# Kernel optimization log

Hardware: AMD Instinct MI355X
Metric: run time of the kernel (lower is better)

The kernel has to match this reference:

```python
import jax, jax.numpy as jnp
import numpy as np

HIDDEN = 512
B, H, W = 8, 48, 48
SCALE = 1.0 / np.sqrt(HIDDEN).astype(np.float32)


def conv1x1(x, w, b):
    # x: [B, C, H, W], w: [O, C], b: [O]  (1x1 Conv2d == channel matmul)
    return jnp.einsum('bchw,oc->bohw', x, w) + b[None, :, None, None]


def setup_inputs() -> dict:
    key = jax.random.key(0)
    ks = jax.random.split(key, 10)
    s = 1.0 / np.sqrt(HIDDEN)
    return {
        'locx': jax.random.normal(ks[0], (B, HIDDEN, H, W), dtype=jnp.float32),
        'glox': jax.random.normal(ks[1], (B, HIDDEN, H, W), dtype=jnp.float32),
        'Wq': jax.random.normal(ks[2], (HIDDEN, HIDDEN), dtype=jnp.float32) * s,
        'bq': jax.random.normal(ks[3], (HIDDEN,), dtype=jnp.float32) * 0.01,
        'Wk': jax.random.normal(ks[4], (HIDDEN, HIDDEN), dtype=jnp.float32) * s,
        'bk': jax.random.normal(ks[5], (HIDDEN,), dtype=jnp.float32) * 0.01,
        'Wv': jax.random.normal(ks[6], (HIDDEN, HIDDEN), dtype=jnp.float32) * s,
        'bv': jax.random.normal(ks[7], (HIDDEN,), dtype=jnp.float32) * 0.01,
        'Wo': jax.random.normal(ks[8], (HIDDEN, HIDDEN), dtype=jnp.float32) * s,
        'bo': jax.random.normal(ks[9], (HIDDEN,), dtype=jnp.float32) * 0.01,
    }


def reference(locx, glox, Wq, bq, Wk, bk, Wv, bv, Wo, bo):
    b, c, h, w = locx.shape
    # 1x1 conv projections
    q = conv1x1(locx, Wq, bq).reshape(b, c, h * w)   # [B, C, N]
    k = conv1x1(glox, Wk, bk).reshape(b, c, -1)      # [B, C, M]
    v = conv1x1(glox, Wv, bv).reshape(b, c, -1)      # [B, C, M]
    # scores = Q^T K / sqrt(hidden)  -> [B, N, M]
    scores = jnp.einsum('bcn,bcm->bnm', q, k) * SCALE
    probs = jax.nn.softmax(scores, axis=-1)           # dropout rate 0.0 -> identity
    # context = probs @ V^T -> [B, N, C] -> [B, C, H, H]
    ctx = jnp.einsum('bnm,bcm->bcn', probs, v).reshape(b, c, h, h)
    out = conv1x1(ctx, Wo, bo)                        # proj dropout 0.0 -> identity
    return out
```

## Files before the change

kernel.cpp:

```cpp
#include <hip/hip_runtime.h>
#include <hip/hip_bf16.h>

typedef __attribute__((ext_vector_type(4))) float f32x4;
typedef __attribute__((ext_vector_type(8))) short bf16x8;
typedef __attribute__((ext_vector_type(4))) short s16x4;

#define C_DIM 512
#define N_PIX 2304
#define N_BATCH 8
#define ATT_SCALE 0.04419417382415922f
#define NJB 9

typedef __attribute__((address_space(3))) unsigned int lds_u32;
typedef const __attribute__((address_space(1))) unsigned int glob_u32;

__device__ __forceinline__ void gl2lds16(const __hip_bfloat16* g, __hip_bfloat16* l)
{
    __builtin_amdgcn_global_load_lds((glob_u32*)g, (lds_u32*)l, 16, 0, 0);
}


#define BAR()  __builtin_amdgcn_s_barrier()
#define LGK0() asm volatile("s_waitcnt lgkmcnt(0)" ::: "memory")
#define VM4()  asm volatile("s_waitcnt vmcnt(4)" ::: "memory")
#define VM0()  asm volatile("s_waitcnt vmcnt(0)" ::: "memory")
#define PRIO(p) __builtin_amdgcn_s_setprio(p)

#define STAGE_A(dd, hh, tk) do { \
    _Pragma("unroll") \
    for (int ss = 0; ss < 2; ++ss) { \
        const int ur0 = wave * 16 + ss * 8; \
        const int row0 = ((ur0 >> 6) << 7) + (hh) * 64 + (ur0 & 63); \
        gl2lds16(gA + (size_t)row0 * C_DIM + (tk) * 64, \
                 (__hip_bfloat16*)&LA[dd][row0 * 64]); \
    } } while (0)

#define STAGE_B(dd, bb, tk) do { \
    _Pragma("unroll") \
    for (int ss = 0; ss < 2; ++ss) { \
        const int ur0 = wave * 16 + ss * 8; \
        const int row0 = ((ur0 >> 5) << 6) + (bb) * 32 + (ur0 & 31); \
        gl2lds16(gB + (size_t)row0 * C_DIM + (tk) * 64, \
                 (__hip_bfloat16*)&LB[dd][row0 * 64]); \
    } } while (0)

#define LOAD_A(dd, hh) do { \
    _Pragma("unroll") \
    for (int tt = 0; tt < 4; ++tt) { \
        const int rb = (wr * 128 + (hh) * 64 + tt * 16 + fr) * 64; \
        _Pragma("unroll") \
        for (int kk = 0; kk < 2; ++kk) \
            aF[tt][kk] = *(const bf16x8*)(&LA[dd][rb + (((kk * 4 + fq) ^ sw) << 3)]); \
    } } while (0)

#define LOAD_B(dd, bb, dst) do { \
    _Pragma("unroll") \
    for (int s2 = 0; s2 < 2; ++s2) { \
        const int rb = (wc * 64 + (bb) * 32 + s2 * 16 + fr) * 64; \
        _Pragma("unroll") \
        for (int kk = 0; kk < 2; ++kk) \
            dst[s2][kk] = *(const bf16x8*)(&LB[dd][rb + (((kk * 4 + fq) ^ sw) << 3)]); \
    } } while (0)

#define MFMA_Q(HH, BB, bsrc) do { \
    _Pragma("unroll") \
    for (int tt = 0; tt < 4; ++tt) \
    _Pragma("unroll") \
    for (int s2 = 0; s2 < 2; ++s2) \
    _Pragma("unroll") \
    for (int kk = 0; kk < 2; ++kk) \
        acc[(HH) * 4 + tt][(BB) * 2 + s2] = __builtin_amdgcn_mfma_f32_16x16x32_bf16( \
            aF[tt][kk], bsrc[s2][kk], acc[(HH) * 4 + tt][(BB) * 2 + s2], 0, 0, 0); \
    } while (0)

template<int NS>
__global__ __launch_bounds__(512, 2)
void s_vp(const __hip_bfloat16* __restrict__ Qt, const __hip_bfloat16* __restrict__ Kt,
          __hip_bfloat16* __restrict__ Pu, float* __restrict__ rp,
          const __hip_bfloat16* __restrict__ wo, const __hip_bfloat16* __restrict__ Vt,
          __hip_bfloat16* __restrict__ Vp, int bz_off, long sPu)
{
    __shared__ __hip_bfloat16 LA[2][256 * 64];
    __shared__ __hip_bfloat16 LB[2][256 * 64];

    const int lin = blockIdx.x;
    const int bz  = lin % NS + bz_off;
    const int t   = lin / NS;
    const bool is_s = (t < 81);

    int ib, jb;
    const __hip_bfloat16 *A, *B;
    __hip_bfloat16* D;
    const long sQ = (long)N_PIX * C_DIM;
    if (is_s) {
        ib = t / 9; jb = t % 9;
        A = Qt + (size_t)bz * sQ;
        B = Kt + (size_t)bz * sQ;
        D = Pu + (size_t)bz * (size_t)sPu;
    } else {
        int u = t - 81;
        ib = u / 9; jb = u % 9;
        A = wo;
        B = Vt + (size_t)bz * sQ;
        D = Vp + (size_t)bz * sQ;
    }
    const int i0 = ib * 256;
    const int j0 = jb * 256;

    const int tid  = threadIdx.x;
    const int lane = tid & 63;
    const int wave = tid >> 6;

    const int lrow = lane >> 3;
    const int lcs  = (lane & 7) ^ lrow;
    const __hip_bfloat16* gA = A + (size_t)(i0 + lrow) * C_DIM + lcs * 8;
    const __hip_bfloat16* gB = B + (size_t)(j0 + lrow) * C_DIM + lcs * 8;

    const int fr = lane & 15;
    const int fq = lane >> 4;
    const int sw = fr & 7;
    const int wr = wave >> 2;
    const int wc = wave & 3;

    f32x4 acc[8][4];
#pragma unroll
    for (int a = 0; a < 8; ++a)
#pragma unroll
        for (int b = 0; b < 4; ++b)
            acc[a][b] = (f32x4){0.f, 0.f, 0.f, 0.f};

    bf16x8 aF[4][2], bF0[2][2], bF1[2][2];

    STAGE_A(0, 0, 0); STAGE_B(0, 0, 0); STAGE_B(0, 1, 0); STAGE_A(0, 1, 0);
    STAGE_A(1, 0, 1); STAGE_B(1, 1, 1);
    VM4();
    BAR();

    for (int kt = 0; kt < 6; ++kt) {
        const int d = kt & 1, e = d ^ 1;
        LOAD_A(d, 0); LOAD_B(d, 0, bF0);
        STAGE_A(e, 1, kt + 1);
        BAR(); LGK0();
        PRIO(1); MFMA_Q(0, 0, bF0); PRIO(0);
        BAR();
        LOAD_B(d, 1, bF1);
        STAGE_B(e, 0, kt + 1);
        BAR(); LGK0();
        PRIO(1); MFMA_Q(0, 1, bF1); PRIO(0);
        BAR();
        LOAD_A(d, 1);
        STAGE_A(d, 0, kt + 2);
        BAR(); LGK0();
        PRIO(1); MFMA_Q(1, 1, bF1); PRIO(0);
        BAR();
        STAGE_B(d, 1, kt + 2);
        VM4();
        BAR();
        PRIO(1); MFMA_Q(1, 0, bF0); PRIO(0);
        BAR();
    }
    {
        LOAD_A(0, 0); LOAD_B(0, 0, bF0);
        STAGE_A(1, 1, 7);
        BAR(); LGK0();
        PRIO(1); MFMA_Q(0, 0, bF0); PRIO(0);
        BAR();
        LOAD_B(0, 1, bF1);
        STAGE_B(1, 0, 7);
        BAR(); LGK0();
        PRIO(1); MFMA_Q(0, 1, bF1); PRIO(0);
        BAR();
        LOAD_A(0, 1);
        BAR(); LGK0();
        PRIO(1); MFMA_Q(1, 1, bF1); PRIO(0);
        BAR();
        VM0();
        BAR();
        PRIO(1); MFMA_Q(1, 0, bF0); PRIO(0);
        BAR();
    }
    {
        LOAD_A(1, 0); LOAD_B(1, 0, bF0);
        BAR(); LGK0();
        PRIO(1); MFMA_Q(0, 0, bF0); PRIO(0);
        BAR();
        LOAD_B(1, 1, bF1);
        BAR(); LGK0();
        PRIO(1); MFMA_Q(0, 1, bF1); PRIO(0);
        BAR();
        LOAD_A(1, 1);
        BAR(); LGK0();
        PRIO(1); MFMA_Q(1, 1, bF1); PRIO(0);
        BAR();
        PRIO(1); MFMA_Q(1, 0, bF0); PRIO(0);
    }

    if (is_s) {
        float rpart[8][4];
#pragma unroll
        for (int a = 0; a < 8; ++a)
#pragma unroll
            for (int r = 0; r < 4; ++r)
                rpart[a][r] = 0.f;
#pragma unroll
        for (int a = 0; a < 8; ++a) {
            const int grow = i0 + wr * 128 + a * 16 + fq * 4;
#pragma unroll
            for (int b = 0; b < 4; ++b) {
                const int col = j0 + wc * 64 + b * 16 + fr;
#pragma unroll
                for (int r = 0; r < 4; ++r) {
                    float v = __expf(acc[a][b][r] * ATT_SCALE);
                    rpart[a][r] += v;
                    D[(size_t)(grow + r) * N_PIX + col] = __float2bfloat16(v);
                }
            }
        }
#pragma unroll
        for (int m = 1; m < 16; m <<= 1)
#pragma unroll
            for (int a = 0; a < 8; ++a)
#pragma unroll
                for (int r = 0; r < 4; ++r)
                    rpart[a][r] += __shfl_xor(rpart[a][r], m);
        float* rsl = (float*)&LA[0][0];
        __syncthreads();
        if (fr == 0) {
#pragma unroll
            for (int a = 0; a < 8; ++a)
#pragma unroll
                for (int r = 0; r < 4; ++r)
                    rsl[wave * 128 + a * 16 + fq * 4 + r] = rpart[a][r];
        }
        __syncthreads();
        if (tid < 256) {
            const int wr2 = tid >> 7, rl = tid & 127;
            float s = rsl[(wr2 * 4 + 0) * 128 + rl] + rsl[(wr2 * 4 + 1) * 128 + rl]
                    + rsl[(wr2 * 4 + 2) * 128 + rl] + rsl[(wr2 * 4 + 3) * 128 + rl];
            rp[((size_t)jb * N_BATCH + bz) * N_PIX + i0 + tid] = s;
        }
    } else {
#pragma unroll
        for (int a = 0; a < 8; ++a) {
            const int grow = i0 + wr * 128 + a * 16 + fq * 4;
#pragma unroll
            for (int b = 0; b < 4; ++b) {
                const int col = j0 + wc * 64 + b * 16 + fr;
#pragma unroll
                for (int r = 0; r < 4; ++r)
                    D[(size_t)(grow + r) * N_PIX + col] = __float2bfloat16(acc[a][b][r]);
            }
        }
    }
}

#undef STAGE_A
#undef STAGE_B
#undef LOAD_A
#undef LOAD_B
#undef MFMA_Q
#undef BAR
#undef LGK0
#undef VM4
#undef VM0
#undef PRIO

template<int NS>
__global__ __launch_bounds__(256)
void pv_out(const __hip_bfloat16* __restrict__ Vp, const __hip_bfloat16* __restrict__ Pu,
            float* __restrict__ out, const float* __restrict__ bo,
            const float* __restrict__ rp, int bz_off, long sPu)
{
    __shared__ __hip_bfloat16 As[64 * 64];
    __shared__ __hip_bfloat16 Bs[128 * 64];

    const int lin = blockIdx.x;
    const int bz  = lin % NS + bz_off;
    const int t   = lin / NS;
    const int ib  = t % 8;
    const int jb  = t / 8;
    const int i0  = ib * 64;
    const int j0  = jb * 128;

    const long sCN = (long)C_DIM * N_PIX;
    const __hip_bfloat16* A = Vp + (size_t)bz * sCN;
    const __hip_bfloat16* B = Pu + (size_t)bz * (size_t)sPu;
    float* D = out + (size_t)bz * sCN;

    const int tid  = threadIdx.x;
    const int lane = tid & 63;
    const int wave = tid >> 6;

    const int lrow = lane >> 3;
    const int lcs  = (lane & 7) ^ lrow;
    const __hip_bfloat16* ga = A + (size_t)(i0 + wave * 16 + lrow) * N_PIX + lcs * 8;
    const __hip_bfloat16* gb = B + (size_t)(j0 + wave * 32 + lrow) * N_PIX + lcs * 8;
    __hip_bfloat16* la = As + wave * 16 * 64;
    __hip_bfloat16* lb = Bs + wave * 32 * 64;

    const int fr = lane & 15;
    const int fq = lane >> 4;
    const int sw = fr & 7;
    const int wi = (wave >> 1) * 32;
    const int wj = (wave & 1) * 64;

    f32x4 acc[2][4];
#pragma unroll
    for (int a = 0; a < 2; ++a)
#pragma unroll
        for (int b = 0; b < 4; ++b)
            acc[a][b] = (f32x4){0.f, 0.f, 0.f, 0.f};

    for (int k0 = 0; k0 < N_PIX; k0 += 64) {
#pragma unroll
        for (int ss = 0; ss < 2; ++ss)
            gl2lds16(ga + (size_t)ss * 8 * N_PIX + k0, la + ss * 8 * 64);
#pragma unroll
        for (int ss = 0; ss < 4; ++ss)
            gl2lds16(gb + (size_t)ss * 8 * N_PIX + k0, lb + ss * 8 * 64);
        __syncthreads();

#pragma unroll
        for (int kk = 0; kk < 2; ++kk) {
            bf16x8 af[2], bfr[4];
            const int ca = ((kk * 4 + fq) ^ sw) << 3;
#pragma unroll
            for (int tt = 0; tt < 2; ++tt)
                af[tt]  = *(const bf16x8*)(&As[(wi + tt * 16 + fr) * 64 + ca]);
#pragma unroll
            for (int tt = 0; tt < 4; ++tt)
                bfr[tt] = *(const bf16x8*)(&Bs[(wj + tt * 16 + fr) * 64 + ca]);
#pragma unroll
            for (int a = 0; a < 2; ++a)
#pragma unroll
                for (int b = 0; b < 4; ++b)
                    acc[a][b] = __builtin_amdgcn_mfma_f32_16x16x32_bf16(
                        af[a], bfr[b], acc[a][b], 0, 0, 0);
        }
        __syncthreads();
    }

    const int orow = fq * 4;
    float rjv[4];
#pragma unroll
    for (int b = 0; b < 4; ++b) {
        int j = j0 + wj + b * 16 + fr;
        float s = 0.f;
#pragma unroll
        for (int jj = 0; jj < NJB; ++jj)
            s += rp[((size_t)jj * N_BATCH + bz) * N_PIX + j];
        rjv[b] = 1.f / s;
    }

#pragma unroll
    for (int a = 0; a < 2; ++a) {
        int ibx = i0 + wi + a * 16 + orow;
#pragma unroll
        for (int r = 0; r < 4; ++r) {
            float bi = bo[ibx + r];
#pragma unroll
            for (int b = 0; b < 4; ++b) {
                int j = j0 + wj + b * 16 + fr;
                D[(size_t)(ibx + r) * N_PIX + j] = acc[a][b][r] * rjv[b] + bi;
            }
        }
    }
}

__global__ __launch_bounds__(256)
void proj_qkv(const __hip_bfloat16* __restrict__ Xl,
              const __hip_bfloat16* __restrict__ Xg,
              const __hip_bfloat16* __restrict__ wgt,
              const float* __restrict__ bq, const float* __restrict__ bk,
              const float* __restrict__ bv,
              __hip_bfloat16* __restrict__ QKV)
{
    __shared__ __hip_bfloat16 As[128 * 64];
    __shared__ __hip_bfloat16 Bs[128 * 64];

    const int lin = blockIdx.x;
    const int s   = lin % 24;
    const int bz  = s & 7;
    const int mat = s >> 3;
    const int t   = lin / 24;
    const int j0  = (t & 3) * 128;
    const int i0  = (t >> 2) * 128;

    const __hip_bfloat16* Ab = ((mat == 0) ? Xl : Xg) + (size_t)bz * N_PIX * C_DIM;
    const __hip_bfloat16* Bb = wgt + (size_t)mat * C_DIM * C_DIM;
    const float* bias = (mat == 0) ? bq : (mat == 1) ? bk : bv;
    __hip_bfloat16* D = QKV + ((size_t)mat * N_BATCH + bz) * N_PIX * C_DIM;

    const int tid  = threadIdx.x;
    const int lane = tid & 63;
    const int wave = tid >> 6;

    const int lrow = lane >> 3;
    const int lcs  = (lane & 7) ^ lrow;
    const __hip_bfloat16* ga = Ab + (size_t)(i0 + wave * 32 + lrow) * C_DIM + lcs * 8;
    const __hip_bfloat16* gb = Bb + (size_t)(j0 + wave * 32 + lrow) * C_DIM + lcs * 8;
    __hip_bfloat16* la = As + wave * 32 * 64;
    __hip_bfloat16* lb = Bs + wave * 32 * 64;

    const int fr = lane & 15;
    const int fq = lane >> 4;
    const int sw = fr & 7;
    const int wi = (wave >> 1) * 64;
    const int wj = (wave & 1) * 64;

    f32x4 acc[4][4];
#pragma unroll
    for (int a = 0; a < 4; ++a)
#pragma unroll
        for (int b = 0; b < 4; ++b)
            acc[a][b] = (f32x4){0.f, 0.f, 0.f, 0.f};

    for (int k0 = 0; k0 < C_DIM; k0 += 64) {
#pragma unroll
        for (int ss = 0; ss < 4; ++ss) {
            gl2lds16(ga + (size_t)ss * 8 * C_DIM + k0, la + ss * 8 * 64);
            gl2lds16(gb + (size_t)ss * 8 * C_DIM + k0, lb + ss * 8 * 64);
        }
        __syncthreads();

#pragma unroll
        for (int kk = 0; kk < 2; ++kk) {
            bf16x8 af[4], bfr[4];
            const int ca = ((kk * 4 + fq) ^ sw) << 3;
#pragma unroll
            for (int tt = 0; tt < 4; ++tt) {
                af[tt]  = *(const bf16x8*)(&As[(wi + tt * 16 + fr) * 64 + ca]);
                bfr[tt] = *(const bf16x8*)(&Bs[(wj + tt * 16 + fr) * 64 + ca]);
            }
#pragma unroll
            for (int a = 0; a < 4; ++a)
#pragma unroll
                for (int b = 0; b < 4; ++b)
                    acc[a][b] = __builtin_amdgcn_mfma_f32_16x16x32_bf16(
                        af[a], bfr[b], acc[a][b], 0, 0, 0);
        }
        __syncthreads();
    }

    const int orow = fq * 4;
#pragma unroll
    for (int a = 0; a < 4; ++a) {
        int ibx = i0 + wi + a * 16 + orow;
#pragma unroll
        for (int b = 0; b < 4; ++b) {
            int j = j0 + wj + b * 16 + fr;
            float bj = bias[j];
#pragma unroll
            for (int r = 0; r < 4; ++r)
                D[(size_t)(ibx + r) * C_DIM + j] = __float2bfloat16(acc[a][b][r] + bj);
        }
    }
}

__global__ __launch_bounds__(256)
void prep(const float* __restrict__ locx, const float* __restrict__ glox,
          __hip_bfloat16* __restrict__ Xl, __hip_bfloat16* __restrict__ Xg,
          const float* __restrict__ w0, const float* __restrict__ w1,
          const float* __restrict__ w2, const float* __restrict__ w3,
          __hip_bfloat16* __restrict__ wgt)
{
    const int lin = blockIdx.x;
    const int tid = threadIdx.x;

    if (lin < 4608) {
        __shared__ float t[64 * 65];
        const int z  = lin & 15;
        const int t2 = lin >> 4;
        const int c0 = (t2 & 7) * 64;
        const int n0 = (t2 >> 3) * 64;
        const size_t b = z & 7;
        const float* Xb = ((z < 8) ? locx : glox) + b * (size_t)C_DIM * N_PIX;
        __hip_bfloat16* Xt = (z < 8) ? Xl : Xg;

        const int n_l = tid & 63;
        const int c_b = tid >> 6;
#pragma unroll
        for (int s = 0; s < 16; ++s) {
            int c_l = c_b + s * 4;
            t[c_l * 65 + n_l] = Xb[(size_t)(c0 + c_l) * N_PIX + n0 + n_l];
        }
        __syncthreads();

        const int cc = (tid & 7) * 8;
        const int nb = tid >> 3;
#pragma unroll
        for (int it = 0; it < 2; ++it) {
            int n2 = nb + it * 32;
            union { __hip_bfloat16 h[8]; int4 v; } u;
#pragma unroll
            for (int w = 0; w < 8; ++w)
                u.h[w] = __float2bfloat16(t[(cc + w) * 65 + n2]);
            *(int4*)(&Xt[(b * N_PIX + n0 + n2) * C_DIM + c0 + cc]) = u.v;
        }
    } else {
        const int idx = lin - 4608;
        const int w   = idx >> 8;
        const float* srcs[4] = {w0, w1, w2, w3};
        const int i = ((idx & 255) * 256 + tid) * 4;
        float4 f = *(const float4*)(srcs[w] + i);
        union { __hip_bfloat16 h[4]; s16x4 q; } u;
        u.h[0] = __float2bfloat16(f.x);
        u.h[1] = __float2bfloat16(f.y);
        u.h[2] = __float2bfloat16(f.z);
        u.h[3] = __float2bfloat16(f.w);
        *(s16x4*)(wgt + (size_t)w * C_DIM * C_DIM + i) = u.q;
    }
}

extern "C" void kernel_launch(void* const* d_in, const int* in_sizes, int n_in,
                              void* d_out, int out_size, void* d_ws, size_t ws_size,
                              hipStream_t stream)
{
    const float* locx = (const float*)d_in[0];
    const float* glox = (const float*)d_in[1];
    const float* Wq = (const float*)d_in[2];
    const float* bq = (const float*)d_in[3];
    const float* Wk = (const float*)d_in[4];
    const float* bk = (const float*)d_in[5];
    const float* Wv = (const float*)d_in[6];
    const float* bv = (const float*)d_in[7];
    const float* Wo = (const float*)d_in[8];
    const float* bo = (const float*)d_in[9];
    float* out = (float*)d_out;

    const int C = C_DIM, N = N_PIX;
    const size_t WB   = (size_t)C * C * 2;
    const size_t szX  = (size_t)N_BATCH * N * C * 2;
    const size_t szP1 = (size_t)N * N * 2;
    const size_t szRP = (size_t)NJB * N_BATCH * N * 4;

    const size_t fixed = 4 * WB + 6 * szX + szRP;
    bool full = (ws_size >= fixed + 8 * szP1 + 4096);

    char* ws = (char*)d_ws;
    size_t off = 0;
    auto alloc = [&](size_t bytes) {
        char* p = ws + off;
        off += (bytes + 255) & ~(size_t)255;
        return p;
    };
    __hip_bfloat16* wgt = (__hip_bfloat16*)alloc(4 * WB);
    __hip_bfloat16* Xl  = (__hip_bfloat16*)alloc(szX);
    __hip_bfloat16* Xg  = (__hip_bfloat16*)alloc(szX);
    __hip_bfloat16* QKV = (__hip_bfloat16*)alloc(3 * szX);
    __hip_bfloat16* Vp  = (__hip_bfloat16*)alloc(szX);
    float*          rp  = (float*)alloc(szRP);
    __hip_bfloat16* Pu  = (__hip_bfloat16*)alloc(full ? 8 * szP1 : szP1);

    __hip_bfloat16* Qt = QKV;
    __hip_bfloat16* Kt = QKV + (size_t)N_BATCH * N * C;
    __hip_bfloat16* Vt = QKV + 2 * (size_t)N_BATCH * N * C;
    __hip_bfloat16* wo_b = wgt + 3 * (size_t)C * C;

    const dim3 blk(256);

    prep<<<dim3(5632), blk, 0, stream>>>(locx, glox, Xl, Xg, Wq, Wk, Wv, Wo, wgt);
    proj_qkv<<<dim3(24 * 72), blk, 0, stream>>>(Xl, Xg, wgt, bq, bk, bv, QKV);

    if (full) {
        s_vp<8><<<dim3(8 * 99), dim3(512), 0, stream>>>(
            Qt, Kt, Pu, rp, wo_b, Vt, Vp, 0, (long)N * N);
        pv_out<8><<<dim3(8 * 144), blk, 0, stream>>>(
            Vp, Pu, out, bo, rp, 0, (long)N * N);
    } else {
        for (int r = 0; r < N_BATCH; ++r) {
            s_vp<1><<<dim3(99), dim3(512), 0, stream>>>(
                Qt, Kt, Pu, rp, wo_b, Vt, Vp, r, 0);
            pv_out<1><<<dim3(144), blk, 0, stream>>>(
                Vp, Pu, out, bo, rp, r, 0);
        }
    }
}
```

Measured before the change: 322.8 us.

## Load A operand directly into registers and simplify GEMM pipeline barriers

The fused score/value-projection GEMM kernel no longer stages the A operand (Q or Wo) through LDS. Each wave now reads its A fragments straight from global memory into double-buffered registers, while only B keeps the LDS double buffer. The main loop is reorganized to one wait and barrier per k-tile instead of several per quarter-step. This halves LDS use and removes barriers, but the four waves sharing a row block now load the same A data redundantly with less coalesced access, and the extra A registers raise pressure under the 512-thread launch bound.

Result: slower. 403.1 us (+24.9%).

```diff
diff --git a/kernel.cpp b/kernel.cpp
--- a/kernel.cpp
+++ b/kernel.cpp
@@ -21,19 +21,8 @@
 
 
 #define BAR()  __builtin_amdgcn_s_barrier()
-#define LGK0() asm volatile("s_waitcnt lgkmcnt(0)" ::: "memory")
-#define VM4()  asm volatile("s_waitcnt vmcnt(4)" ::: "memory")
 #define VM0()  asm volatile("s_waitcnt vmcnt(0)" ::: "memory")
 #define PRIO(p) __builtin_amdgcn_s_setprio(p)
-
-#define STAGE_A(dd, hh, tk) do { \
-    _Pragma("unroll") \
-    for (int ss = 0; ss < 2; ++ss) { \
-        const int ur0 = wave * 16 + ss * 8; \
-        const int row0 = ((ur0 >> 6) << 7) + (hh) * 64 + (ur0 & 63); \
-        gl2lds16(gA + (size_t)row0 * C_DIM + (tk) * 64, \
-                 (__hip_bfloat16*)&LA[dd][row0 * 64]); \
-    } } while (0)
 
 #define STAGE_B(dd, bb, tk) do { \
     _Pragma("unroll") \
@@ -44,25 +33,25 @@
                  (__hip_bfloat16*)&LB[dd][row0 * 64]); \
     } } while (0)
 
-#define LOAD_A(dd, hh) do { \
-    _Pragma("unroll") \
-    for (int tt = 0; tt < 4; ++tt) { \
-        const int rb = (wr * 128 + (hh) * 64 + tt * 16 + fr) * 64; \
-        _Pragma("unroll") \
-        for (int kk = 0; kk < 2; ++kk) \
-            aF[tt][kk] = *(const bf16x8*)(&LA[dd][rb + (((kk * 4 + fq) ^ sw) << 3)]); \
-    } } while (0)
-
-#define LOAD_B(dd, bb, dst) do { \
+#define RD_B(dd, bb) do { \
     _Pragma("unroll") \
     for (int s2 = 0; s2 < 2; ++s2) { \
         const int rb = (wc * 64 + (bb) * 32 + s2 * 16 + fr) * 64; \
         _Pragma("unroll") \
         for (int kk = 0; kk < 2; ++kk) \
-            dst[s2][kk] = *(const bf16x8*)(&LB[dd][rb + (((kk * 4 + fq) ^ sw) << 3)]); \
+            bF[s2][kk] = *(const bf16x8*)(&LB[dd][rb + (((kk * 4 + fq) ^ sw) << 3)]); \
     } } while (0)
 
-#define MFMA_Q(HH, BB, bsrc) do { \
+#define LD_A(dst, hh, tk) do { \
+    _Pragma("unroll") \
+    for (int tt = 0; tt < 4; ++tt) { \
+        _Pragma("unroll") \
+        for (int kk = 0; kk < 2; ++kk) \
+            dst[tt][kk] = *(const bf16x8*)(gAf + \
+                (size_t)((hh) * 64 + tt * 16) * C_DIM + (tk) * 64 + kk * 32); \
+    } } while (0)
+
+#define MFMA_Q(HH, BB, asrc) do { PRIO(1); \
     _Pragma("unroll") \
     for (int tt = 0; tt < 4; ++tt) \
     _Pragma("unroll") \
@@ -70,8 +59,8 @@
     _Pragma("unroll") \
     for (int kk = 0; kk < 2; ++kk) \
         acc[(HH) * 4 + tt][(BB) * 2 + s2] = __builtin_amdgcn_mfma_f32_16x16x32_bf16( \
-            aF[tt][kk], bsrc[s2][kk], acc[(HH) * 4 + tt][(BB) * 2 + s2], 0, 0, 0); \
-    } while (0)
+            asrc[tt][kk], bF[s2][kk], acc[(HH) * 4 + tt][(BB) * 2 + s2], 0, 0, 0); \
+    PRIO(0); } while (0)
 
 template<int NS>
 __global__ __launch_bounds__(512, 2)
@@ -80,7 +69,6 @@
           const __hip_bfloat16* __restrict__ wo, const __hip_bfloat16* __restrict__ Vt,
           __hip_bfloat16* __restrict__ Vp, int bz_off, long sPu)
 {
-    __shared__ __hip_bfloat16 LA[2][256 * 64];
     __shared__ __hip_bfloat16 LB[2][256 * 64];
 
     const int lin = blockIdx.x;
@@ -113,7 +101,6 @@
 
     const int lrow = lane >> 3;
     const int lcs  = (lane & 7) ^ lrow;
-    const __hip_bfloat16* gA = A + (size_t)(i0 + lrow) * C_DIM + lcs * 8;
     const __hip_bfloat16* gB = B + (size_t)(j0 + lrow) * C_DIM + lcs * 8;
 
     const int fr = lane & 15;
@@ -122,6 +109,8 @@
     const int wr = wave >> 2;
     const int wc = wave & 3;
 
+    const __hip_bfloat16* gAf = A + (size_t)(i0 + wr * 128 + fr) * C_DIM + fq * 8;
+
     f32x4 acc[8][4];
 #pragma unroll
     for (int a = 0; a < 8; ++a)
@@ -129,70 +118,39 @@
         for (int b = 0; b < 4; ++b)
             acc[a][b] = (f32x4){0.f, 0.f, 0.f, 0.f};
 
-    bf16x8 aF[4][2], bF0[2][2], bF1[2][2];
-
-    STAGE_A(0, 0, 0); STAGE_B(0, 0, 0); STAGE_B(0, 1, 0); STAGE_A(0, 1, 0);
-    STAGE_A(1, 0, 1); STAGE_B(1, 1, 1);
-    VM4();
+    bf16x8 aH0[4][2], aH1[4][2], bF[2][2];
+
+    STAGE_B(0, 0, 0); STAGE_B(0, 1, 0);
+    LD_A(aH0, 0, 0);
+    VM0();
     BAR();
 
-    for (int kt = 0; kt < 6; ++kt) {
+#pragma unroll
+    for (int kt = 0; kt < 7; ++kt) {
         const int d = kt & 1, e = d ^ 1;
-        LOAD_A(d, 0); LOAD_B(d, 0, bF0);
-        STAGE_A(e, 1, kt + 1);
-        BAR(); LGK0();
-        PRIO(1); MFMA_Q(0, 0, bF0); PRIO(0);
-        BAR();
-        LOAD_B(d, 1, bF1);
+        RD_B(d, 0);
         STAGE_B(e, 0, kt + 1);
-        BAR(); LGK0();
-        PRIO(1); MFMA_Q(0, 1, bF1); PRIO(0);
-        BAR();
-        LOAD_A(d, 1);
-        STAGE_A(d, 0, kt + 2);
-        BAR(); LGK0();
-        PRIO(1); MFMA_Q(1, 1, bF1); PRIO(0);
-        BAR();
-        STAGE_B(d, 1, kt + 2);
-        VM4();
-        BAR();
-        PRIO(1); MFMA_Q(1, 0, bF0); PRIO(0);
-        BAR();
-    }
-    {
-        LOAD_A(0, 0); LOAD_B(0, 0, bF0);
-        STAGE_A(1, 1, 7);
-        BAR(); LGK0();
-        PRIO(1); MFMA_Q(0, 0, bF0); PRIO(0);
-        BAR();
-        LOAD_B(0, 1, bF1);
-        STAGE_B(1, 0, 7);
-        BAR(); LGK0();
-        PRIO(1); MFMA_Q(0, 1, bF1); PRIO(0);
-        BAR();
-        LOAD_A(0, 1);
-        BAR(); LGK0();
-        PRIO(1); MFMA_Q(1, 1, bF1); PRIO(0);
-        BAR();
+        STAGE_B(e, 1, kt + 1);
+        LD_A(aH1, 1, kt);
+        MFMA_Q(0, 0, aH0);
+        RD_B(d, 1);
+        MFMA_Q(0, 1, aH0);
+        LD_A(aH0, 0, kt + 1);
+        MFMA_Q(1, 1, aH1);
+        RD_B(d, 0);
+        MFMA_Q(1, 0, aH1);
         VM0();
         BAR();
-        PRIO(1); MFMA_Q(1, 0, bF0); PRIO(0);
-        BAR();
     }
     {
-        LOAD_A(1, 0); LOAD_B(1, 0, bF0);
-        BAR(); LGK0();
-        PRIO(1); MFMA_Q(0, 0, bF0); PRIO(0);
-        BAR();
-        LOAD_B(1, 1, bF1);
-        BAR(); LGK0();
-        PRIO(1); MFMA_Q(0, 1, bF1); PRIO(0);
-        BAR();
-        LOAD_A(1, 1);
-        BAR(); LGK0();
-        PRIO(1); MFMA_Q(1, 1, bF1); PRIO(0);
-        BAR();
-        PRIO(1); MFMA_Q(1, 0, bF0); PRIO(0);
+        RD_B(1, 0);
+        LD_A(aH1, 1, 7);
+        MFMA_Q(0, 0, aH0);
+        RD_B(1, 1);
+        MFMA_Q(0, 1, aH0);
+        MFMA_Q(1, 1, aH1);
+        RD_B(1, 0);
+        MFMA_Q(1, 0, aH1);
     }
 
     if (is_s) {
@@ -223,8 +181,7 @@
 #pragma unroll
                 for (int r = 0; r < 4; ++r)
                     rpart[a][r] += __shfl_xor(rpart[a][r], m);
-        float* rsl = (float*)&LA[0][0];
-        __syncthreads();
+        float* rsl = (float*)&LB[0][0];
         if (fr == 0) {
 #pragma unroll
             for (int a = 0; a < 8; ++a)
@@ -254,14 +211,11 @@
     }
 }
 
-#undef STAGE_A
 #undef STAGE_B
-#undef LOAD_A
-#undef LOAD_B
+#undef RD_B
+#undef LD_A
 #undef MFMA_Q
 #undef BAR
-#undef LGK0
-#undef VM4
 #undef VM0
 #undef PRIO
 
```

## Double-buffer LDS tiles in pv_out and proj_qkv GEMM main loops

Applied to the files above, without the earlier changes.

Both GEMM kernels move from a single LDS buffer to two ping-pong buffers. Each iteration issues the async global-to-LDS loads for the next K tile before running the MFMAs on the current one. This hides global load latency behind compute and replaces two __syncthreads per tile with one vmcnt wait plus one barrier. In exchange, LDS use per block doubles (48 KB for pv_out, 64 KB for proj_qkv), which may lower occupancy.

Result: slower. 329.6 us (+2.1%).

```diff
diff --git a/kernel.cpp b/kernel.cpp
--- a/kernel.cpp
+++ b/kernel.cpp
@@ -18,6 +18,9 @@
 {
     __builtin_amdgcn_global_load_lds((glob_u32*)g, (lds_u32*)l, 16, 0, 0);
 }
+
+#define GBAR() __builtin_amdgcn_s_barrier()
+#define GVM0() asm volatile("s_waitcnt vmcnt(0)" ::: "memory")
 
 
 #define BAR()  __builtin_amdgcn_s_barrier()
@@ -265,14 +268,45 @@
 #undef VM0
 #undef PRIO
 
+
+#define PV_STAGE(ee, tk) do { \
+    _Pragma("unroll") \
+    for (int ss = 0; ss < 2; ++ss) \
+        gl2lds16(ga + (size_t)ss * 8 * N_PIX + (tk) * 64, \
+                 laA + (ee) * (64 * 64) + ss * 8 * 64); \
+    _Pragma("unroll") \
+    for (int ss = 0; ss < 4; ++ss) \
+        gl2lds16(gb + (size_t)ss * 8 * N_PIX + (tk) * 64, \
+                 laB + (ee) * (128 * 64) + ss * 8 * 64); \
+    } while (0)
+
+#define PV_COMP(dd) do { \
+    _Pragma("unroll") \
+    for (int kk = 0; kk < 2; ++kk) { \
+        bf16x8 af[2], bfr[4]; \
+        const int ca = ((kk * 4 + fq) ^ sw) << 3; \
+        _Pragma("unroll") \
+        for (int tt = 0; tt < 2; ++tt) \
+            af[tt]  = *(const bf16x8*)(&As[dd][(wi + tt * 16 + fr) * 64 + ca]); \
+        _Pragma("unroll") \
+        for (int tt = 0; tt < 4; ++tt) \
+            bfr[tt] = *(const bf16x8*)(&Bs[dd][(wj + tt * 16 + fr) * 64 + ca]); \
+        _Pragma("unroll") \
+        for (int a = 0; a < 2; ++a) \
+        _Pragma("unroll") \
+        for (int b = 0; b < 4; ++b) \
+            acc[a][b] = __builtin_amdgcn_mfma_f32_16x16x32_bf16( \
+                af[a], bfr[b], acc[a][b], 0, 0, 0); \
+    } } while (0)
+
 template<int NS>
 __global__ __launch_bounds__(256)
 void pv_out(const __hip_bfloat16* __restrict__ Vp, const __hip_bfloat16* __restrict__ Pu,
             float* __restrict__ out, const float* __restrict__ bo,
             const float* __restrict__ rp, int bz_off, long sPu)
 {
-    __shared__ __hip_bfloat16 As[64 * 64];
-    __shared__ __hip_bfloat16 Bs[128 * 64];
+    __shared__ __hip_bfloat16 As[2][64 * 64];
+    __shared__ __hip_bfloat16 Bs[2][128 * 64];
 
     const int lin = blockIdx.x;
     const int bz  = lin % NS + bz_off;
@@ -295,8 +329,8 @@
     const int lcs  = (lane & 7) ^ lrow;
     const __hip_bfloat16* ga = A + (size_t)(i0 + wave * 16 + lrow) * N_PIX + lcs * 8;
     const __hip_bfloat16* gb = B + (size_t)(j0 + wave * 32 + lrow) * N_PIX + lcs * 8;
-    __hip_bfloat16* la = As + wave * 16 * 64;
-    __hip_bfloat16* lb = Bs + wave * 32 * 64;
+    __hip_bfloat16* laA = &As[0][wave * 16 * 64];
+    __hip_bfloat16* laB = &Bs[0][wave * 32 * 64];
 
     const int fr = lane & 15;
     const int fq = lane >> 4;
@@ -311,34 +345,22 @@
         for (int b = 0; b < 4; ++b)
             acc[a][b] = (f32x4){0.f, 0.f, 0.f, 0.f};
 
-    for (int k0 = 0; k0 < N_PIX; k0 += 64) {
-#pragma unroll
-        for (int ss = 0; ss < 2; ++ss)
-            gl2lds16(ga + (size_t)ss * 8 * N_PIX + k0, la + ss * 8 * 64);
-#pragma unroll
-        for (int ss = 0; ss < 4; ++ss)
-            gl2lds16(gb + (size_t)ss * 8 * N_PIX + k0, lb + ss * 8 * 64);
-        __syncthreads();
-
-#pragma unroll
-        for (int kk = 0; kk < 2; ++kk) {
-            bf16x8 af[2], bfr[4];
-            const int ca = ((kk * 4 + fq) ^ sw) << 3;
-#pragma unroll
-            for (int tt = 0; tt < 2; ++tt)
-                af[tt]  = *(const bf16x8*)(&As[(wi + tt * 16 + fr) * 64 + ca]);
-#pragma unroll
-            for (int tt = 0; tt < 4; ++tt)
-                bfr[tt] = *(const bf16x8*)(&Bs[(wj + tt * 16 + fr) * 64 + ca]);
-#pragma unroll
-            for (int a = 0; a < 2; ++a)
-#pragma unroll
-                for (int b = 0; b < 4; ++b)
-                    acc[a][b] = __builtin_amdgcn_mfma_f32_16x16x32_bf16(
-                        af[a], bfr[b], acc[a][b], 0, 0, 0);
-        }
-        __syncthreads();
-    }
+    PV_STAGE(0, 0);
+    GVM0(); GBAR();
+
+#pragma unroll 1
+    for (int kt = 0; kt < 34; kt += 2) {
+        PV_STAGE(1, kt + 1);
+        PV_COMP(0);
+        GVM0(); GBAR();
+        PV_STAGE(0, kt + 2);
+        PV_COMP(1);
+        GVM0(); GBAR();
+    }
+    PV_STAGE(1, 35);
+    PV_COMP(0);
+    GVM0(); GBAR();
+    PV_COMP(1);
 
     const int orow = fq * 4;
     float rjv[4];
@@ -366,6 +388,37 @@
         }
     }
 }
+
+#undef PV_STAGE
+#undef PV_COMP
+
+
+#define PJ_STAGE(ee, tk) do { \
+    _Pragma("unroll") \
+    for (int ss = 0; ss < 4; ++ss) { \
+        gl2lds16(ga + (size_t)ss * 8 * C_DIM + (tk) * 64, \
+                 laA + (ee) * (128 * 64) + ss * 8 * 64); \
+        gl2lds16(gb + (size_t)ss * 8 * C_DIM + (tk) * 64, \
+                 laB + (ee) * (128 * 64) + ss * 8 * 64); \
+    } } while (0)
+
+#define PJ_COMP(dd) do { \
+    _Pragma("unroll") \
+    for (int kk = 0; kk < 2; ++kk) { \
+        bf16x8 af[4], bfr[4]; \
+        const int ca = ((kk * 4 + fq) ^ sw) << 3; \
+        _Pragma("unroll") \
+        for (int tt = 0; tt < 4; ++tt) { \
+            af[tt]  = *(const bf16x8*)(&As[dd][(wi + tt * 16 + fr) * 64 + ca]); \
+            bfr[tt] = *(const bf16x8*)(&Bs[dd][(wj + tt * 16 + fr) * 64 + ca]); \
+        } \
+        _Pragma("unroll") \
+        for (int a = 0; a < 4; ++a) \
+        _Pragma("unroll") \
+        for (int b = 0; b < 4; ++b) \
+            acc[a][b] = __builtin_amdgcn_mfma_f32_16x16x32_bf16( \
+                af[a], bfr[b], acc[a][b], 0, 0, 0); \
+    } } while (0)
 
 __global__ __launch_bounds__(256)
 void proj_qkv(const __hip_bfloat16* __restrict__ Xl,
@@ -375,8 +428,8 @@
               const float* __restrict__ bv,
               __hip_bfloat16* __restrict__ QKV)
 {
-    __shared__ __hip_bfloat16 As[128 * 64];
-    __shared__ __hip_bfloat16 Bs[128 * 64];
+    __shared__ __hip_bfloat16 As[2][128 * 64];
+    __shared__ __hip_bfloat16 Bs[2][128 * 64];
 
     const int lin = blockIdx.x;
     const int s   = lin % 24;
@@ -399,8 +452,8 @@
     const int lcs  = (lane & 7) ^ lrow;
     const __hip_bfloat16* ga = Ab + (size_t)(i0 + wave * 32 + lrow) * C_DIM + lcs * 8;
     const __hip_bfloat16* gb = Bb + (size_t)(j0 + wave * 32 + lrow) * C_DIM + lcs * 8;
-    __hip_bfloat16* la = As + wave * 32 * 64;
-    __hip_bfloat16* lb = Bs + wave * 32 * 64;
+    __hip_bfloat16* laA = &As[0][wave * 32 * 64];
+    __hip_bfloat16* laB = &Bs[0][wave * 32 * 64];
 
     const int fr = lane & 15;
     const int fq = lane >> 4;
@@ -415,32 +468,22 @@
         for (int b = 0; b < 4; ++b)
             acc[a][b] = (f32x4){0.f, 0.f, 0.f, 0.f};
 
-    for (int k0 = 0; k0 < C_DIM; k0 += 64) {
-#pragma unroll
-        for (int ss = 0; ss < 4; ++ss) {
-            gl2lds16(ga + (size_t)ss * 8 * C_DIM + k0, la + ss * 8 * 64);
-            gl2lds16(gb + (size_t)ss * 8 * C_DIM + k0, lb + ss * 8 * 64);
-        }
-        __syncthreads();
-
-#pragma unroll
-        for (int kk = 0; kk < 2; ++kk) {
-            bf16x8 af[4], bfr[4];
-            const int ca = ((kk * 4 + fq) ^ sw) << 3;
-#pragma unroll
-            for (int tt = 0; tt < 4; ++tt) {
-                af[tt]  = *(const bf16x8*)(&As[(wi + tt * 16 + fr) * 64 + ca]);
-                bfr[tt] = *(const bf16x8*)(&Bs[(wj + tt * 16 + fr) * 64 + ca]);
-            }
-#pragma unroll
-            for (int a = 0; a < 4; ++a)
-#pragma unroll
-                for (int b = 0; b < 4; ++b)
-                    acc[a][b] = __builtin_amdgcn_mfma_f32_16x16x32_bf16(
-                        af[a], bfr[b], acc[a][b], 0, 0, 0);
-        }
-        __syncthreads();
-    }
+    PJ_STAGE(0, 0);
+    GVM0(); GBAR();
+
+#pragma unroll 1
+    for (int kt = 0; kt < 6; kt += 2) {
+        PJ_STAGE(1, kt + 1);
+        PJ_COMP(0);
+        GVM0(); GBAR();
+        PJ_STAGE(0, kt + 2);
+        PJ_COMP(1);
+        GVM0(); GBAR();
+    }
+    PJ_STAGE(1, 7);
+    PJ_COMP(0);
+    GVM0(); GBAR();
+    PJ_COMP(1);
 
     const int orow = fq * 4;
 #pragma unroll
@@ -456,6 +499,9 @@
         }
     }
 }
+
+#undef PJ_STAGE
+#undef PJ_COMP
 
 __global__ __launch_bounds__(256)
 void prep(const float* __restrict__ locx, const float* __restrict__ glox,
```
